# Optimization experiments

Hardware: AMD Instinct MI355X
Metric: run time of the kernel (lower is better)

The kernel has to match this reference:

```python
import jax, jax.numpy as jnp
import numpy as np

IN, OUT, HID = 64, 32, 256
B, T = 64, 256
NOISE_STD, TAU = 0.05, 0.2


def setup_inputs() -> dict:
    key = jax.random.key(0)
    ks = jax.random.split(key, 8)
    u = jax.random.normal(ks[0], (B, T, IN), dtype=jnp.float32)
    x0 = jax.random.normal(ks[1], (B, HID), dtype=jnp.float32)
    noise = jax.random.normal(ks[2], (T, B, HID), dtype=jnp.float32)
    w_hh_rnn = jax.random.normal(ks[3], (HID, HID), dtype=jnp.float32) * (0.1 / HID ** 0.5)
    w_hh_tbrnn = jax.random.normal(ks[4], (HID, HID, HID), dtype=jnp.float32) * (0.1 / HID)
    w_in_w = jax.random.normal(ks[5], (HID, IN), dtype=jnp.float32)
    w_in_b = jnp.zeros((HID,), dtype=jnp.float32)
    w_out_w = jax.random.normal(ks[6], (OUT, HID), dtype=jnp.float32) * 4.0
    w_out_b = jax.random.normal(ks[7], (OUT,), dtype=jnp.float32) * 0.0
    return {"u": u, "x0": x0, "noise": noise, "w_hh_rnn": w_hh_rnn,
            "w_hh_tbrnn": w_hh_tbrnn, "w_in_w": w_in_w, "w_in_b": w_in_b,
            "w_out_w": w_out_w, "w_out_b": w_out_b}


def reference(u, x0, noise, w_hh_rnn, w_hh_tbrnn, w_in_w, w_in_b, w_out_w, w_out_b):
    # mode='cont', form='rate', adv=False, nonlinearity=tanh, output_nonlinearity=tanh
    u_t_first = jnp.transpose(u, (1, 0, 2))  # [T, B, IN]

    def step(x, inp):
        u_t, n_t = inp
        r = jnp.tanh(x)                                   # rate form
        input_I = u_t @ w_in_w.T + w_in_b                 # [B, HID]
        hidden_W1 = r @ w_hh_rnn.T                        # [B, HID]
        # out[b,j] = sum_{i,k} r[b,i] * W[j,i,k] * r[b,k]
        hidden_W2 = jnp.einsum('bi,jik,bk->bj', r, w_hh_tbrnn, r)
        rec_x = hidden_W1 + hidden_W2 + input_I
        x_new = x + NOISE_STD * n_t + TAU * (-x + rec_x)  # cont mode
        return x_new, x_new

    x_final, traj = jax.lax.scan(step, x0, (u_t_first, noise))
    trajectories = jnp.transpose(traj, (1, 0, 2))         # [B, T, HID]
    output = jnp.tanh(trajectories) @ w_out_w.T + w_out_b  # [B, T, OUT]
    return output, x_final, trajectories
```

## Files before the change

kernel.cpp:

```cpp
#include <hip/hip_runtime.h>
#include <hip/hip_bf16.h>
#include <math.h>

#define HID 256
#define BSZ 64
#define TLEN 256
#define INW 64
#define OUTW 32
#define NOISE_STD 0.05f
#define TAU 0.2f

typedef __attribute__((ext_vector_type(8))) short short8;
typedef __attribute__((ext_vector_type(4))) short shortx4;
typedef __attribute__((ext_vector_type(4))) float floatx4;
typedef unsigned long long u64;

__device__ __forceinline__ int ridx(int b, int k) {
    int P = ((b >> 2) & 7) ^ ((b & 3) << 1);
    return b * 256 + ((((k >> 3) ^ P) & 31) << 3) + (k & 7);
}

__device__ __forceinline__ float fast_tanh(float x) {
    float e = __expf(2.f * x);
    return 1.f - 2.f / (e + 1.f);
}

__global__ __launch_bounds__(256) void swizzle_kernel(const float* __restrict__ W,
                                                      __hip_bfloat16* __restrict__ Wsw) {
    int g = blockIdx.x * 256 + threadIdx.x;
    int l  = g & 63;
    int ni = (g >> 6) & 15;
    int kk = (g >> 10) & 7;
    int j  = g >> 13;
    int i  = ni * 16 + (l & 15);
    int k0 = kk * 32 + (l >> 4) * 8;
    const float* __restrict__ src = W + ((size_t)j * HID + i) * HID + k0;
    __hip_bfloat16* __restrict__ dst = Wsw + (size_t)g * 8;
#pragma unroll
    for (int e = 0; e < 8; ++e) dst[e] = __float2bfloat16(src[e]);
}

__global__ __launch_bounds__(256) void init_kernel(const float* __restrict__ x0,
                                                   u64* __restrict__ buf0) {
    int g = blockIdx.x;
    int k = threadIdx.x;
    u64 v = 0;
#pragma unroll
    for (int e = 0; e < 4; ++e) {
        __hip_bfloat16 h = __float2bfloat16(tanhf(x0[(4 * g + e) * HID + k]));
        v |= (u64)(*(unsigned short*)&h) << (16 * e);
    }
    buf0[g * 256 + k] = v;
}

__global__ __launch_bounds__(256) void pre_kernel(const float* __restrict__ u,
                                                  const float* __restrict__ w_in_w,
                                                  const float* __restrict__ w_in_b,
                                                  const float* __restrict__ noise,
                                                  float* __restrict__ pre) {
    __shared__ float ulds[BSZ][INW + 4];
    const int t = blockIdx.x;
    const int j = threadIdx.x;
    {
        int b = threadIdx.x >> 2, q = threadIdx.x & 3;
#pragma unroll
        for (int e = 0; e < 4; ++e) {
            float4 v = *(const float4*)(u + ((size_t)b * TLEN + t) * INW + q * 16 + e * 4);
            *(float4*)&ulds[b][q * 16 + e * 4] = v;
        }
    }
    float wreg[INW];
#pragma unroll
    for (int q = 0; q < INW / 4; ++q) {
        float4 v = *(const float4*)(w_in_w + (size_t)j * INW + q * 4);
        wreg[q * 4 + 0] = v.x; wreg[q * 4 + 1] = v.y;
        wreg[q * 4 + 2] = v.z; wreg[q * 4 + 3] = v.w;
    }
    float bias = w_in_b[j];
    __syncthreads();
    for (int b = 0; b < BSZ; ++b) {
        float s = bias;
#pragma unroll
        for (int in_ = 0; in_ < INW; ++in_) s = fmaf(ulds[b][in_], wreg[in_], s);
        float nz = noise[((size_t)t * BSZ + b) * HID + j];
        pre[((size_t)t * HID + j) * BSZ + b] = NOISE_STD * nz + TAU * s;
    }
}

__global__ __launch_bounds__(256, 1) void persist_kernel(
    const __hip_bfloat16* __restrict__ Wsw,
    const float* __restrict__ w_hh,
    const float* __restrict__ u,
    const float* __restrict__ w_in_w,
    const float* __restrict__ w_in_b,
    const float* __restrict__ noise,
    const float* __restrict__ x0,
    u64* __restrict__ buf0,
    u64* __restrict__ buf1,
    float* __restrict__ traj,
    float* __restrict__ trajWS,
    float* __restrict__ xfinal,
    int* __restrict__ ready,
    const float* __restrict__ pre,
    int use_pre, int use_tws) {
    __shared__ short rlds[16384];
    __shared__ float redw[256];
    __shared__ float exl[2][64];

    const int tid  = threadIdx.x;
    const int j    = blockIdx.x;
    const int w    = tid >> 6;
    const int lane = tid & 63;
    const int quad = lane >> 4;
    const int col  = lane & 15;

    short8 wreg[32];
    {
        const short* __restrict__ wsh = (const short*)Wsw;
#pragma unroll
        for (int kk = 0; kk < 8; ++kk)
#pragma unroll
            for (int mt = 0; mt < 4; ++mt)
                wreg[kk * 4 + mt] = *(const short8*)(wsh +
                    ((((size_t)j * 8 + kk) * 16 + (w * 4 + mt)) * 64 + lane) * 8);
    }
    float whh16[16];
#pragma unroll
    for (int mt = 0; mt < 4; ++mt)
#pragma unroll
        for (int rg = 0; rg < 4; ++rg)
            whh16[mt * 4 + rg] = w_hh[j * HID + (w * 4 + mt) * 16 + quad * 4 + rg];

    float xb = 0.f;
    if (tid < 128) xb = x0[lane * HID + j];

#pragma unroll 1
    for (int t = 0; t < TLEN; ++t) {
        const u64* __restrict__ rcur = (t & 1) ? buf1 : buf0;
        u64* __restrict__ rnxt = (t & 1) ? buf0 : buf1;

        float extra = 0.f;
        if (tid < BSZ) {
            if (use_pre) {
                extra = pre[((size_t)t * HID + j) * BSZ + tid];
            } else {
                float isum = w_in_b[j];
                const float4* __restrict__ urow =
                    (const float4*)(u + ((size_t)tid * TLEN + t) * INW);
                const float4* __restrict__ wrow = (const float4*)(w_in_w + (size_t)j * INW);
#pragma unroll
                for (int q = 0; q < INW / 4; ++q) {
                    float4 uu = urow[q], ww = wrow[q];
                    isum = fmaf(uu.x, ww.x, isum);
                    isum = fmaf(uu.y, ww.y, isum);
                    isum = fmaf(uu.z, ww.z, isum);
                    isum = fmaf(uu.w, ww.w, isum);
                }
                float nz = noise[((size_t)t * BSZ + tid) * HID + j];
                extra = NOISE_STD * nz + TAU * isum;
            }
            exl[t & 1][tid] = extra;
        }

        if (t > 0) {
            while (__hip_atomic_load(ready + tid * 16, __ATOMIC_RELAXED,
                                     __HIP_MEMORY_SCOPE_AGENT) < t)
                __builtin_amdgcn_s_sleep(1);
            asm volatile("" ::: "memory");
        }

        {
            u64 v[16];
#pragma unroll
            for (int g = 0; g < 16; ++g)
                v[g] = __hip_atomic_load(rcur + g * 256 + tid, __ATOMIC_RELAXED,
                                         __HIP_MEMORY_SCOPE_AGENT);
#pragma unroll
            for (int g = 0; g < 16; ++g)
#pragma unroll
                for (int e = 0; e < 4; ++e)
                    rlds[ridx(4 * g + e, tid)] = (short)(v[g] >> (16 * e));
        }
        __syncthreads();

        float ex_w1 = 0.f;
        if (w == 1) ex_w1 = exl[t & 1][lane];

        floatx4 acc[4][4];
#pragma unroll
        for (int mt = 0; mt < 4; ++mt)
#pragma unroll
            for (int nt = 0; nt < 4; ++nt)
                acc[mt][nt] = (floatx4){whh16[mt * 4 + 0], whh16[mt * 4 + 1],
                                        whh16[mt * 4 + 2], whh16[mt * 4 + 3]};

#pragma unroll
        for (int kk = 0; kk < 8; ++kk) {
            short8 afrag[4];
#pragma unroll
            for (int nt = 0; nt < 4; ++nt)
                afrag[nt] = *(const short8*)&rlds[ridx(nt * 16 + col, kk * 32 + quad * 8)];
#pragma unroll
            for (int mt = 0; mt < 4; ++mt)
#pragma unroll
                for (int nt = 0; nt < 4; ++nt)
                    acc[mt][nt] = __builtin_amdgcn_mfma_f32_16x16x32_bf16(
                        wreg[kk * 4 + mt], afrag[nt], acc[mt][nt], 0, 0, 0);
        }

        float part[4];
#pragma unroll
        for (int nt = 0; nt < 4; ++nt) part[nt] = 0.f;
#pragma unroll
        for (int mt = 0; mt < 4; ++mt) {
            const int ib = (w * 4 + mt) * 16 + quad * 4;
#pragma unroll
            for (int nt = 0; nt < 4; ++nt) {
                const int b = nt * 16 + col;
                shortx4 r4 = *(const shortx4*)&rlds[ridx(b, ib)];
#pragma unroll
                for (int rg = 0; rg < 4; ++rg) {
                    short rs = r4[rg];
                    float rv = __bfloat162float(*(__hip_bfloat16*)&rs);
                    part[nt] = fmaf(rv, acc[mt][nt][rg], part[nt]);
                }
            }
        }
#pragma unroll
        for (int nt = 0; nt < 4; ++nt) {
            part[nt] += __shfl_xor(part[nt], 16, 64);
            part[nt] += __shfl_xor(part[nt], 32, 64);
        }
        if (quad == 0) {
#pragma unroll
            for (int nt = 0; nt < 4; ++nt)
                redw[(nt * 16 + col) * 4 + w] = part[nt];
        }
        __syncthreads();

        if (w < 2) {
            const int b = lane;
            float4 r4 = *(const float4*)&redw[b * 4];
            float rec = (r4.x + r4.y) + (r4.z + r4.w);
            float ex = (w == 0) ? extra : ex_w1;
            float xn = xb + ex + TAU * (rec - xb);
            xb = xn;

            if (w == 1) {
                if (t < TLEN - 1) {
                    __hip_bfloat16 h = __float2bfloat16(fast_tanh(xn));
                    int hs = (int)(*(unsigned short*)&h);
                    int src = 4 * (lane & 15);
                    u64 pv = (u64)(unsigned)__shfl(hs, src + 0, 64)
                           | ((u64)(unsigned)__shfl(hs, src + 1, 64) << 16)
                           | ((u64)(unsigned)__shfl(hs, src + 2, 64) << 32)
                           | ((u64)(unsigned)__shfl(hs, src + 3, 64) << 48);
                    if (lane < 16)
                        __hip_atomic_store(rnxt + (size_t)lane * 256 + j, pv,
                                           __ATOMIC_RELAXED, __HIP_MEMORY_SCOPE_AGENT);
                    asm volatile("s_waitcnt vmcnt(0)" ::: "memory");
                    if (lane == 0)
                        __hip_atomic_store(ready + j * 16, t + 1, __ATOMIC_RELAXED,
                                           __HIP_MEMORY_SCOPE_AGENT);
                    asm volatile("s_waitcnt vmcnt(0)" ::: "memory");
                }
            } else {
                if (use_tws) {
                    trajWS[((size_t)t * HID + j) * BSZ + b] = xn;
                } else {
                    traj[((size_t)b * TLEN + t) * HID + j] = xn;
                    if (t == TLEN - 1) xfinal[b * HID + j] = xn;
                }
                asm volatile("s_waitcnt vmcnt(0)" ::: "memory");
            }
        }
    }
}

__global__ __launch_bounds__(256) void fixup_kernel(
    const float* __restrict__ trajWS,
    const float* __restrict__ w_out_w,
    const float* __restrict__ w_out_b,
    float* __restrict__ traj,
    float* __restrict__ xfinal,
    float* __restrict__ out) {
    __shared__ float xv[BSZ * 257];
    __shared__ float wol[OUTW * 257];
    const int t = blockIdx.x, tid = threadIdx.x;

#pragma unroll
    for (int it = 0; it < 16; ++it) {
        int flat = it * 1024 + tid * 4;
        float4 v = *(const float4*)(trajWS + (size_t)t * 16384 + flat);
        int jj = flat >> 6, b = flat & 63;
        xv[(b + 0) * 257 + jj] = v.x;
        xv[(b + 1) * 257 + jj] = v.y;
        xv[(b + 2) * 257 + jj] = v.z;
        xv[(b + 3) * 257 + jj] = v.w;
    }
#pragma unroll
    for (int it = 0; it < 8; ++it) {
        int flat = it * 1024 + tid * 4;
        float4 v = *(const float4*)(w_out_w + flat);
        int o = flat >> 8, h = flat & 255;
        *(float4*)&wol[o * 257 + h] = v;
    }
    __syncthreads();

    for (int b = 0; b < BSZ; ++b)
        traj[((size_t)b * TLEN + t) * HID + tid] = xv[b * 257 + tid];
    if (t == TLEN - 1)
        for (int b = 0; b < BSZ; ++b)
            xfinal[b * HID + tid] = xv[b * 257 + tid];

    __syncthreads();
#pragma unroll
    for (int it = 0; it < 64; ++it)
        xv[it * 257 + tid] = tanhf(xv[it * 257 + tid]);
    __syncthreads();

    const int o = tid & 31;
    const float bias = w_out_b[o];
#pragma unroll 1
    for (int rep = 0; rep < 8; ++rep) {
        int b = rep * 8 + (tid >> 5);
        float s = bias;
#pragma unroll 8
        for (int h = 0; h < HID; ++h)
            s = fmaf(xv[b * 257 + h], wol[o * 257 + h], s);
        out[((size_t)b * TLEN + t) * OUTW + o] = s;
    }
}

__global__ __launch_bounds__(256) void output_kernel(
    const float* __restrict__ traj, const float* __restrict__ w_out_w,
    const float* __restrict__ w_out_b, float* __restrict__ out) {
    __shared__ float th[8][HID + 1];
    const int bt0 = blockIdx.x * 8;
    const int tid = threadIdx.x;
#pragma unroll
    for (int m = 0; m < 8; ++m) {
        int idx = m * 256 + tid;
        th[idx >> 8][idx & 255] = tanhf(traj[(size_t)bt0 * HID + idx]);
    }
    __syncthreads();
    const int row = tid >> 5, o = tid & 31;
    const float* __restrict__ wrow = w_out_w + (size_t)o * HID;
    float s = w_out_b[o];
#pragma unroll 8
    for (int h = 0; h < HID; ++h) s = fmaf(th[row][h], wrow[h], s);
    out[(size_t)(bt0 + row) * OUTW + o] = s;
}

extern "C" void kernel_launch(void* const* d_in, const int* in_sizes, int n_in,
                              void* d_out, int out_size, void* d_ws, size_t ws_size,
                              hipStream_t stream) {
    const float* u       = (const float*)d_in[0];
    const float* x0      = (const float*)d_in[1];
    const float* noise   = (const float*)d_in[2];
    const float* w_hh    = (const float*)d_in[3];
    const float* W       = (const float*)d_in[4];
    const float* w_in_w  = (const float*)d_in[5];
    const float* w_in_b  = (const float*)d_in[6];
    const float* w_out_w = (const float*)d_in[7];
    const float* w_out_b = (const float*)d_in[8];

    float* out    = (float*)d_out;
    float* xfinal = out + (size_t)BSZ * TLEN * OUTW;
    float* traj   = xfinal + (size_t)BSZ * HID;

    char* ws = (char*)d_ws;
    __hip_bfloat16* Wsw = (__hip_bfloat16*)ws;
    u64*   buf0 = (u64*)(ws + 33554432);
    u64*   buf1 = (u64*)(ws + 33587200);
    int*   rdy  = (int*)(ws + 33619968);
    float* tws  = (float*)(ws + 33636352);
    float* pre  = (float*)(ws + 50413568);
    const size_t NEED_TWS = 50413568ull;
    const size_t NEED_PRE = 67190784ull;
    const int use_tws = (ws_size >= NEED_TWS) ? 1 : 0;
    const int use_pre = (ws_size >= NEED_PRE) ? 1 : 0;

    hipMemsetAsync(rdy, 0, 16384, stream);
    swizzle_kernel<<<8192, 256, 0, stream>>>(W, Wsw);
    init_kernel<<<16, 256, 0, stream>>>(x0, buf0);
    if (use_pre)
        pre_kernel<<<TLEN, 256, 0, stream>>>(u, w_in_w, w_in_b, noise, pre);

    persist_kernel<<<256, 256, 0, stream>>>(
        Wsw, w_hh, u, w_in_w, w_in_b, noise, x0,
        buf0, buf1, traj, tws, xfinal, rdy, pre, use_pre, use_tws);

    if (use_tws)
        fixup_kernel<<<TLEN, 256, 0, stream>>>(tws, w_out_w, w_out_b, traj, xfinal, out);
    else
        output_kernel<<<(BSZ * TLEN) / 8, 256, 0, stream>>>(traj, w_out_w, w_out_b, out);
}
```

Before: 1.444 ms.

## Fuse weight swizzle into persistent kernel prologue and merge init into pre kernel

Removes the separate swizzle kernel that converted the 64 MB fp32 third-order weight into a bf16 swizzled workspace copy. Each persistent block now loads its slice of the fp32 weight directly, converts it to bf16 and keeps it in registers. The init step is folded into the first 16 blocks of pre_kernel, which drops one launch, and the workspace layout shrinks. In exchange, the persistent kernel's prologue reads twice as many bytes with strided float4 loads.

```diff
diff --git a/kernel.cpp b/kernel.cpp
--- a/kernel.cpp
+++ b/kernel.cpp
@@ -25,25 +25,8 @@
     return 1.f - 2.f / (e + 1.f);
 }
 
-__global__ __launch_bounds__(256) void swizzle_kernel(const float* __restrict__ W,
-                                                      __hip_bfloat16* __restrict__ Wsw) {
-    int g = blockIdx.x * 256 + threadIdx.x;
-    int l  = g & 63;
-    int ni = (g >> 6) & 15;
-    int kk = (g >> 10) & 7;
-    int j  = g >> 13;
-    int i  = ni * 16 + (l & 15);
-    int k0 = kk * 32 + (l >> 4) * 8;
-    const float* __restrict__ src = W + ((size_t)j * HID + i) * HID + k0;
-    __hip_bfloat16* __restrict__ dst = Wsw + (size_t)g * 8;
-#pragma unroll
-    for (int e = 0; e < 8; ++e) dst[e] = __float2bfloat16(src[e]);
-}
-
-__global__ __launch_bounds__(256) void init_kernel(const float* __restrict__ x0,
-                                                   u64* __restrict__ buf0) {
-    int g = blockIdx.x;
-    int k = threadIdx.x;
+__device__ __forceinline__ void init_body(const float* __restrict__ x0,
+                                          u64* __restrict__ buf0, int g, int k) {
     u64 v = 0;
 #pragma unroll
     for (int e = 0; e < 4; ++e) {
@@ -51,16 +34,24 @@
         v |= (u64)(*(unsigned short*)&h) << (16 * e);
     }
     buf0[g * 256 + k] = v;
+}
+
+__global__ __launch_bounds__(256) void init_kernel(const float* __restrict__ x0,
+                                                   u64* __restrict__ buf0) {
+    init_body(x0, buf0, blockIdx.x, threadIdx.x);
 }
 
 __global__ __launch_bounds__(256) void pre_kernel(const float* __restrict__ u,
                                                   const float* __restrict__ w_in_w,
                                                   const float* __restrict__ w_in_b,
                                                   const float* __restrict__ noise,
-                                                  float* __restrict__ pre) {
+                                                  float* __restrict__ pre,
+                                                  const float* __restrict__ x0,
+                                                  u64* __restrict__ buf0) {
     __shared__ float ulds[BSZ][INW + 4];
     const int t = blockIdx.x;
     const int j = threadIdx.x;
+    if (t < 16) init_body(x0, buf0, t, j);
     {
         int b = threadIdx.x >> 2, q = threadIdx.x & 3;
 #pragma unroll
@@ -88,7 +79,7 @@
 }
 
 __global__ __launch_bounds__(256, 1) void persist_kernel(
-    const __hip_bfloat16* __restrict__ Wsw,
+    const float* __restrict__ W,
     const float* __restrict__ w_hh,
     const float* __restrict__ u,
     const float* __restrict__ w_in_w,
@@ -116,13 +107,27 @@
 
     short8 wreg[32];
     {
-        const short* __restrict__ wsh = (const short*)Wsw;
+        const float* __restrict__ wsrc = W + (size_t)j * HID * HID;
 #pragma unroll
         for (int kk = 0; kk < 8; ++kk)
 #pragma unroll
-            for (int mt = 0; mt < 4; ++mt)
-                wreg[kk * 4 + mt] = *(const short8*)(wsh +
-                    ((((size_t)j * 8 + kk) * 16 + (w * 4 + mt)) * 64 + lane) * 8);
+            for (int mt = 0; mt < 4; ++mt) {
+                const float* __restrict__ p =
+                    wsrc + (size_t)((w * 4 + mt) * 16 + col) * HID + kk * 32 + quad * 8;
+                float4 f0 = *(const float4*)p;
+                float4 f1 = *(const float4*)(p + 4);
+                short8 s;
+                __hip_bfloat16 h;
+                h = __float2bfloat16(f0.x); s[0] = *(short*)&h;
+                h = __float2bfloat16(f0.y); s[1] = *(short*)&h;
+                h = __float2bfloat16(f0.z); s[2] = *(short*)&h;
+                h = __float2bfloat16(f0.w); s[3] = *(short*)&h;
+                h = __float2bfloat16(f1.x); s[4] = *(short*)&h;
+                h = __float2bfloat16(f1.y); s[5] = *(short*)&h;
+                h = __float2bfloat16(f1.z); s[6] = *(short*)&h;
+                h = __float2bfloat16(f1.w); s[7] = *(short*)&h;
+                wreg[kk * 4 + mt] = s;
+            }
     }
     float whh16[16];
 #pragma unroll
@@ -370,25 +375,24 @@
     float* traj   = xfinal + (size_t)BSZ * HID;
 
     char* ws = (char*)d_ws;
-    __hip_bfloat16* Wsw = (__hip_bfloat16*)ws;
-    u64*   buf0 = (u64*)(ws + 33554432);
-    u64*   buf1 = (u64*)(ws + 33587200);
-    int*   rdy  = (int*)(ws + 33619968);
-    float* tws  = (float*)(ws + 33636352);
-    float* pre  = (float*)(ws + 50413568);
-    const size_t NEED_TWS = 50413568ull;
-    const size_t NEED_PRE = 67190784ull;
+    u64*   buf0 = (u64*)ws;
+    u64*   buf1 = (u64*)(ws + 32768);
+    int*   rdy  = (int*)(ws + 65536);
+    float* tws  = (float*)(ws + 81920);
+    float* pre  = (float*)(ws + 16859136);
+    const size_t NEED_TWS = 16859136ull;
+    const size_t NEED_PRE = 33636352ull;
     const int use_tws = (ws_size >= NEED_TWS) ? 1 : 0;
     const int use_pre = (ws_size >= NEED_PRE) ? 1 : 0;
 
     hipMemsetAsync(rdy, 0, 16384, stream);
-    swizzle_kernel<<<8192, 256, 0, stream>>>(W, Wsw);
-    init_kernel<<<16, 256, 0, stream>>>(x0, buf0);
     if (use_pre)
-        pre_kernel<<<TLEN, 256, 0, stream>>>(u, w_in_w, w_in_b, noise, pre);
+        pre_kernel<<<TLEN, 256, 0, stream>>>(u, w_in_w, w_in_b, noise, pre, x0, buf0);
+    else
+        init_kernel<<<16, 256, 0, stream>>>(x0, buf0);
 
     persist_kernel<<<256, 256, 0, stream>>>(
-        Wsw, w_hh, u, w_in_w, w_in_b, noise, x0,
+        W, w_hh, u, w_in_w, w_in_b, noise, x0,
         buf0, buf1, traj, tws, xfinal, rdy, pre, use_pre, use_tws);
 
     if (use_tws)
```

Result: no change. 1.439 ms (-0.3%).
